# Performance work log

Hardware: AMD Instinct MI355X
Metric: run time of the kernel (lower is better)

## Reference

```python
import jax, jax.numpy as jnp
import numpy as np
from jax import lax

B, L, T = 200000, 64, 16  # symbols, input length (== filter_size), channel taps


def _conv1d(x, w, stride):
    # x: [N, Cin, L], w: [Cout, Cin, K] -> [N, Cout, Lout]; lax conv = correlation (matches torch)
    return lax.conv_general_dilated(x, w, (stride,), 'VALID',
                                    dimension_numbers=('NCH', 'OIH', 'NCH'))


def setup_inputs() -> dict:
    key = jax.random.key(0)
    ks = jax.random.split(key, 7)
    return {
        'x': jax.random.normal(ks[0], (B, 2, L), dtype=jnp.float32),
        'conv1_w': jax.random.normal(ks[1], (1, 2, L // 4), dtype=jnp.float32) * 0.1,
        'conv1_b': jax.random.normal(ks[2], (1,), dtype=jnp.float32) * 0.1,
        'conv2_w': jax.random.normal(ks[3], (2, 1, 4), dtype=jnp.float32) * 0.1,
        'conv2_b': jax.random.normal(ks[4], (2,), dtype=jnp.float32) * 0.1,
        'taps_real': jax.random.normal(ks[5], (T,), dtype=jnp.float32),
        'taps_imag': jax.random.normal(ks[6], (T,), dtype=jnp.float32),
    }


def reference(x, conv1_w, conv1_b, conv2_w, conv2_b, taps_real, taps_imag):
    k1 = conv1_w.shape[2]  # filter_size // 4; stride == kernel
    h = jax.nn.elu(_conv1d(x, conv1_w, k1) + conv1_b[None, :, None])   # [B,1,4]
    rst = jax.nn.elu(_conv1d(h, conv2_w, 1) + conv2_b[None, :, None])  # [B,2,1]

    nT = taps_real.shape[0]
    sr = rst[:, 0, 0]  # real sequence over the batch/time axis, [B]
    si = rst[:, 1, 0]
    pr = jnp.pad(sr, (nT - 1, 0))  # causal zero padding, as torch.cat(zeros, rst)
    pi = jnp.pad(si, (nT - 1, 0))
    # torch code correlates windows with flipped taps -> use flipped taps as corr kernel
    hr = jnp.flip(taps_real)
    hi = jnp.flip(taps_imag)

    def corr(sig, ker):
        return lax.conv_general_dilated(sig[None, None, :], ker[None, None, :], (1,),
                                        'VALID', dimension_numbers=('NCH', 'OIH', 'NCH'))[0, 0]

    y_real = corr(pr, hr) - corr(pi, hi)  # [B]
    y_imag = corr(pr, hi) + corr(pi, hr)
    return jnp.stack([y_real, y_imag], axis=1)[:, :, None]  # [B,2,1]
```

## Files before the change

### kernel.cpp

```cpp
#include <hip/hip_runtime.h>
#include <math.h>

#define BLOCK 1024
#define EPB 240
#define TAPS 16
#define HWIN 16

__device__ __forceinline__ float eluf(float v) { return v > 0.f ? v : expm1f(v); }
__device__ __forceinline__ float dot4(float4 a, float4 b) {
    return a.x * b.x + a.y * b.y + a.z * b.z + a.w * b.w;
}

__device__ __forceinline__ void conv_elem(const float4* __restrict__ xf4, long ge,
        int j, float4 wv0, float4 wv1, float b1s,
        const float* __restrict__ w2, float b20, float b21,
        float& sr, float& si)
{
    const float4* base = xf4 + ge * 32;
    float4 v0 = base[j],      v1 = base[4 + j],
           v2 = base[8 + j],  v3 = base[12 + j];
    float a0 = dot4(v0, wv0), a1 = dot4(v1, wv0),
          a2 = dot4(v2, wv0), a3 = dot4(v3, wv0);
    v0 = base[16 + j]; v1 = base[20 + j]; v2 = base[24 + j]; v3 = base[28 + j];
    a0 += dot4(v0, wv1); a1 += dot4(v1, wv1);
    a2 += dot4(v2, wv1); a3 += dot4(v3, wv1);

    a0 += __shfl_xor(a0, 1); a1 += __shfl_xor(a1, 1);
    a2 += __shfl_xor(a2, 1); a3 += __shfl_xor(a3, 1);
    a0 += __shfl_xor(a0, 2); a1 += __shfl_xor(a1, 2);
    a2 += __shfl_xor(a2, 2); a3 += __shfl_xor(a3, 2);

    float h0 = eluf(a0 + b1s), h1 = eluf(a1 + b1s);
    float h2 = eluf(a2 + b1s), h3 = eluf(a3 + b1s);

    float pr = b20 + h0 * w2[0] + h1 * w2[1] + h2 * w2[2] + h3 * w2[3];
    float pi = b21 + h0 * w2[4] + h1 * w2[5] + h2 * w2[6] + h3 * w2[7];
    sr = eluf(pr);
    si = eluf(pi);
}

__global__ __launch_bounds__(BLOCK, 8) void NF_20581483282566_kernel(
    const float* __restrict__ x,
    const float* __restrict__ w1, const float* __restrict__ b1,
    const float* __restrict__ w2, const float* __restrict__ b2,
    const float* __restrict__ tr, const float* __restrict__ ti,
    float2* __restrict__ out, int B)
{
    __shared__ float s_r[HWIN + EPB];
    __shared__ float s_i[HWIN + EPB];

    const int t = threadIdx.x;
    const int j = t & 3;
    const long b0 = (long)blockIdx.x * EPB;

    const float4* xf4 = reinterpret_cast<const float4*>(x);
    const float4* w1v = reinterpret_cast<const float4*>(w1);
    const float4 wv0 = w1v[j];
    const float4 wv1 = w1v[4 + j];
    const float b1s = b1[0];
    const float b20 = b2[0], b21 = b2[1];

    if (t < 4 * EPB) {
        const int e_loc = t >> 2;
        const long ge = b0 + e_loc;
        if (ge < B) {
            float sr, si;
            conv_elem(xf4, ge, j, wv0, wv1, b1s, w2, b20, b21, sr, si);
            if (j == 0) { s_r[HWIN + e_loc] = sr; s_i[HWIN + e_loc] = si; }
        }
    } else {
        const int eh = (t - 4 * EPB) >> 2;
        const long he = b0 - HWIN + eh;
        float sr = 0.f, si = 0.f;
        if (he >= 0)
            conv_elem(xf4, he, j, wv0, wv1, b1s, w2, b20, b21, sr, si);
        if (j == 0) { s_r[eh] = sr; s_i[eh] = si; }
    }
    __syncthreads();

    if (t < EPB) {
        const long b = b0 + t;
        if (b < B) {
            float yr = 0.f, yi = 0.f;
#pragma unroll
            for (int jj = 0; jj < TAPS; ++jj) {
                float a = s_r[HWIN + t - jj];
                float c = s_i[HWIN + t - jj];
                float trj = tr[jj], tij = ti[jj];
                yr += a * trj - c * tij;
                yi += a * tij + c * trj;
            }
            out[b] = make_float2(yr, yi);
        }
    }
}

extern "C" void kernel_launch(void* const* d_in, const int* in_sizes, int n_in,
                              void* d_out, int out_size, void* d_ws, size_t ws_size,
                              hipStream_t stream) {
    const float* x  = (const float*)d_in[0];
    const float* w1 = (const float*)d_in[1];
    const float* b1 = (const float*)d_in[2];
    const float* w2 = (const float*)d_in[3];
    const float* b2 = (const float*)d_in[4];
    const float* tr = (const float*)d_in[5];
    const float* ti = (const float*)d_in[6];
    float2* out = (float2*)d_out;

    const int B = in_sizes[0] / 128;
    const int grid = (B + EPB - 1) / EPB;
    NF_20581483282566_kernel<<<grid, BLOCK, 0, stream>>>(x, w1, b1, w2, b2, tr, ti, out, B);
}
```

Before: 23.63 us.

## Split fused conv+FIR kernel into separate conv and FIR kernels via workspace

Replaces the single fused kernel, which recomputed a 16-element halo of conv outputs per block, with two kernels. The first computes the conv/ELU stage per symbol and writes complex samples to a workspace buffer. The second loads tiles plus halo from that buffer and applies the 16-tap complex FIR. This drops the halo recomputation and the large 1024-thread blocks, at the cost of an extra launch and a round trip of the intermediate through global memory.

```diff
diff --git a/kernel.cpp b/kernel.cpp
--- a/kernel.cpp
+++ b/kernel.cpp
@@ -1,21 +1,32 @@
 #include <hip/hip_runtime.h>
 #include <math.h>
 
-#define BLOCK 1024
-#define EPB 240
 #define TAPS 16
-#define HWIN 16
+#define HALO (TAPS - 1)
+#define K2_EPB 256
 
 __device__ __forceinline__ float eluf(float v) { return v > 0.f ? v : expm1f(v); }
 __device__ __forceinline__ float dot4(float4 a, float4 b) {
     return a.x * b.x + a.y * b.y + a.z * b.z + a.w * b.w;
 }
 
-__device__ __forceinline__ void conv_elem(const float4* __restrict__ xf4, long ge,
-        int j, float4 wv0, float4 wv1, float b1s,
-        const float* __restrict__ w2, float b20, float b21,
-        float& sr, float& si)
+__global__ __launch_bounds__(256, 8) void NF_conv_kernel(
+    const float* __restrict__ x,
+    const float* __restrict__ w1, const float* __restrict__ b1,
+    const float* __restrict__ w2, const float* __restrict__ b2,
+    float2* __restrict__ s, int B)
 {
+    const int t = threadIdx.x;
+    const int j = t & 3;
+    const long ge = (long)blockIdx.x * 64 + (t >> 2);
+
+    const float4* xf4 = reinterpret_cast<const float4*>(x);
+    const float4* w1v = reinterpret_cast<const float4*>(w1);
+    const float4 wv0 = w1v[j];
+    const float4 wv1 = w1v[4 + j];
+
+    if (ge >= B) return;
+
     const float4* base = xf4 + ge * 32;
     float4 v0 = base[j],      v1 = base[4 + j],
            v2 = base[8 + j],  v3 = base[12 + j];
@@ -30,68 +41,50 @@
     a0 += __shfl_xor(a0, 2); a1 += __shfl_xor(a1, 2);
     a2 += __shfl_xor(a2, 2); a3 += __shfl_xor(a3, 2);
 
-    float h0 = eluf(a0 + b1s), h1 = eluf(a1 + b1s);
-    float h2 = eluf(a2 + b1s), h3 = eluf(a3 + b1s);
-
-    float pr = b20 + h0 * w2[0] + h1 * w2[1] + h2 * w2[2] + h3 * w2[3];
-    float pi = b21 + h0 * w2[4] + h1 * w2[5] + h2 * w2[6] + h3 * w2[7];
-    sr = eluf(pr);
-    si = eluf(pi);
+    if (j == 0) {
+        const float b1s = b1[0];
+        float h0 = eluf(a0 + b1s), h1 = eluf(a1 + b1s);
+        float h2 = eluf(a2 + b1s), h3 = eluf(a3 + b1s);
+        float pr = b2[0] + h0 * w2[0] + h1 * w2[1] + h2 * w2[2] + h3 * w2[3];
+        float pi = b2[1] + h0 * w2[4] + h1 * w2[5] + h2 * w2[6] + h3 * w2[7];
+        s[ge] = make_float2(eluf(pr), eluf(pi));
+    }
 }
 
-__global__ __launch_bounds__(BLOCK, 8) void NF_20581483282566_kernel(
-    const float* __restrict__ x,
-    const float* __restrict__ w1, const float* __restrict__ b1,
-    const float* __restrict__ w2, const float* __restrict__ b2,
+__global__ __launch_bounds__(256) void NF_fir_kernel(
+    const float2* __restrict__ s,
     const float* __restrict__ tr, const float* __restrict__ ti,
     float2* __restrict__ out, int B)
 {
-    __shared__ float s_r[HWIN + EPB];
-    __shared__ float s_i[HWIN + EPB];
+    __shared__ float s_r[K2_EPB + HALO];
+    __shared__ float s_i[K2_EPB + HALO];
 
     const int t = threadIdx.x;
-    const int j = t & 3;
-    const long b0 = (long)blockIdx.x * EPB;
+    const long base = (long)blockIdx.x * K2_EPB;
+    const long b = base + t;
 
-    const float4* xf4 = reinterpret_cast<const float4*>(x);
-    const float4* w1v = reinterpret_cast<const float4*>(w1);
-    const float4 wv0 = w1v[j];
-    const float4 wv1 = w1v[4 + j];
-    const float b1s = b1[0];
-    const float b20 = b2[0], b21 = b2[1];
-
-    if (t < 4 * EPB) {
-        const int e_loc = t >> 2;
-        const long ge = b0 + e_loc;
-        if (ge < B) {
-            float sr, si;
-            conv_elem(xf4, ge, j, wv0, wv1, b1s, w2, b20, b21, sr, si);
-            if (j == 0) { s_r[HWIN + e_loc] = sr; s_i[HWIN + e_loc] = si; }
-        }
-    } else {
-        const int eh = (t - 4 * EPB) >> 2;
-        const long he = b0 - HWIN + eh;
-        float sr = 0.f, si = 0.f;
-        if (he >= 0)
-            conv_elem(xf4, he, j, wv0, wv1, b1s, w2, b20, b21, sr, si);
-        if (j == 0) { s_r[eh] = sr; s_i[eh] = si; }
+    if (t < HALO) {
+        long hb = base - HALO + t;
+        float2 v = (hb >= 0) ? s[hb] : make_float2(0.f, 0.f);
+        s_r[t] = v.x;  s_i[t] = v.y;
+    }
+    {
+        float2 v = (b < B) ? s[b] : make_float2(0.f, 0.f);
+        s_r[HALO + t] = v.x;  s_i[HALO + t] = v.y;
     }
     __syncthreads();
 
-    if (t < EPB) {
-        const long b = b0 + t;
-        if (b < B) {
-            float yr = 0.f, yi = 0.f;
+    if (b < B) {
+        float yr = 0.f, yi = 0.f;
 #pragma unroll
-            for (int jj = 0; jj < TAPS; ++jj) {
-                float a = s_r[HWIN + t - jj];
-                float c = s_i[HWIN + t - jj];
-                float trj = tr[jj], tij = ti[jj];
-                yr += a * trj - c * tij;
-                yi += a * tij + c * trj;
-            }
-            out[b] = make_float2(yr, yi);
+        for (int jj = 0; jj < TAPS; ++jj) {
+            float a = s_r[HALO + t - jj];
+            float c = s_i[HALO + t - jj];
+            float trj = tr[jj], tij = ti[jj];
+            yr += a * trj - c * tij;
+            yi += a * tij + c * trj;
         }
+        out[b] = make_float2(yr, yi);
     }
 }
 
@@ -108,6 +101,11 @@
     float2* out = (float2*)d_out;
 
     const int B = in_sizes[0] / 128;
-    const int grid = (B + EPB - 1) / EPB;
-    NF_20581483282566_kernel<<<grid, BLOCK, 0, stream>>>(x, w1, b1, w2, b2, tr, ti, out, B);
+    float2* s = (float2*)d_ws;
+
+    const int grid1 = (B + 63) / 64;
+    NF_conv_kernel<<<grid1, 256, 0, stream>>>(x, w1, b1, w2, b2, s, B);
+
+    const int grid2 = (B + K2_EPB - 1) / K2_EPB;
+    NF_fir_kernel<<<grid2, 256, 0, stream>>>(s, tr, ti, out, B);
 }
```

Result: slower. 24.35 us (+3.0%).
